# Performance work log

Measured on AMD Instinct MI355X. Metric: run time of the kernel, lower is better.

Reference implementation:

```python
import jax, jax.numpy as jnp
import numpy as np

L, B, S, H = 2, 32, 2048, 256  # layers, batch, seqlen, hidden (=input_size)


def setup_inputs() -> dict:
    key = jax.random.key(0)
    k0, k1, k2, k3, k4 = jax.random.split(key, 5)
    scale = 1.0 / np.sqrt(H)
    inputs = jax.random.normal(k0, (B, S, H), jnp.float32)
    W_ih = jax.random.uniform(k1, (L, 4 * H, H), jnp.float32, -scale, scale)
    b_ih = jax.random.uniform(k2, (L, 4 * H), jnp.float32, -scale, scale)
    W_hh = jax.random.uniform(k3, (L, 4 * H, H), jnp.float32, -scale, scale)
    b_hh = jax.random.uniform(k4, (L, 4 * H), jnp.float32, -scale, scale)
    return {"inputs": inputs, "W_ih": W_ih, "b_ih": b_ih, "W_hh": W_hh, "b_hh": b_hh}


def _lstm_layer(x, Wi, bi, Wh, bh):
    # Precompute input projection for the whole sequence (matches cells[l].ih(prev_layer)).
    xp = jnp.einsum('bsh,gh->bsg', x, Wi) + bi  # [B, S, 4H]
    hid = Wh.shape[1]
    h0 = jnp.zeros((x.shape[0], hid), x.dtype)
    c0 = jnp.zeros((x.shape[0], hid), x.dtype)

    def step(carry, xt):
        h, c = carry
        gates = xt + h @ Wh.T + bh          # [B, 4H]
        i, f, g, o = jnp.split(gates, 4, axis=-1)
        c = jax.nn.sigmoid(f) * c + jax.nn.sigmoid(i) * jnp.tanh(g)
        h = jax.nn.sigmoid(o) * jnpp_tanh(c) if False else jax.nn.sigmoid(o) * jnp.tanh(c)
        return (h, c), h

    (hT, cT), ys = jax.lax.scan(step, (h0, c0), jnp.swapaxes(xp, 0, 1))  # scan over time
    return jnp.swapaxes(ys, 0, 1), hT, cT  # [B, S, H], [B, H], [B, H]


def reference(inputs, W_ih, b_ih, W_hh, b_hh):
    # Eval-mode forward: locked dropout is identity; hiddens initialized to zeros.
    x = inputs
    hs, cs = [], []
    for l in range(W_ih.shape[0]):
        x, hT, cT = _lstm_layer(x, W_ih[l], b_ih[l], W_hh[l], b_hh[l])
        hs.append(hT)
        cs.append(cT)
    # outputs [B,S,H]; final hiddens each [L,B,H]
    return x, jnp.stack(hs, axis=0), jnp.stack(cs, axis=0)
```

## Files before the change

kernel.cpp:

```cpp
#include <hip/hip_runtime.h>
#include <cstdint>
#include <cstddef>

typedef _Float16 half_t;
typedef _Float16 half2_t __attribute__((ext_vector_type(2)));
typedef _Float16 half8_t __attribute__((ext_vector_type(8)));
typedef float   float4_t __attribute__((ext_vector_type(4)));

#define L_N 2
#define B_N 32
#define S_N 2048
#define H_N 256
#define G_N 1024
#define M_N (B_N*S_N)

#define RING_R 4
#define RING_BYTES (B_N*RING_R*128*8)

#define WS_A0   0ull
#define WS_XP   33554432ull
#define WS_WI   167772160ull
#define WS_WH   168820736ull
#define WS_BSUM 169869312ull
#define WS_HP0  169877504ull
#define WS_HP1  170008576ull

__global__ void cvt_f32_f16(const float* __restrict__ in, half_t* __restrict__ out, int n){
  int i = blockIdx.x*256 + threadIdx.x;
  if (i < n) out[i] = (half_t)in[i];
}

__global__ void make_bsum(const float* __restrict__ bi, const float* __restrict__ bh,
                          float* __restrict__ bs, int n){
  int i = blockIdx.x*256 + threadIdx.x;
  if (i < n) bs[i] = bi[i] + bh[i];
}

__global__ __launch_bounds__(256) void gemm_xp(
    const half_t* __restrict__ A, const half_t* __restrict__ W,
    const float* __restrict__ bsum, half_t* __restrict__ XP)
{
  const int wave = threadIdx.x >> 6;
  const int lane = threadIdx.x & 63;
  const int l15 = lane & 15, quad = lane >> 4;
  const int m0 = blockIdx.x*64 + wave*16;
  const int n0 = blockIdx.y*64;
  float4_t acc[4] = {{0,0,0,0},{0,0,0,0},{0,0,0,0},{0,0,0,0}};
  const half_t* arow = A + (size_t)(m0 + l15)*H_N + quad*8;
  const half_t* brow[4];
  #pragma unroll
  for (int nt=0; nt<4; ++nt)
    brow[nt] = W + (size_t)(n0 + nt*16 + l15)*H_N + quad*8;
  #pragma unroll
  for (int k0=0; k0<H_N; k0+=32){
    half8_t af = *(const half8_t*)(arow + k0);
    #pragma unroll
    for (int nt=0; nt<4; ++nt){
      half8_t bf = *(const half8_t*)(brow[nt] + k0);
      acc[nt] = __builtin_amdgcn_mfma_f32_16x16x32_f16(af, bf, acc[nt], 0, 0, 0);
    }
  }
  #pragma unroll
  for (int nt=0; nt<4; ++nt){
    const int col = n0 + nt*16 + l15;
    const int cell = col & 255, gate = col >> 8;
    const float bs = bsum[col];
    #pragma unroll
    for (int r=0; r<4; ++r){
      XP[(size_t)(m0 + quad*4 + r)*G_N + cell*4 + gate] = (half_t)(acc[nt][r] + bs);
    }
  }
}

__device__ __forceinline__ float sigf(float x){ return 1.f/(1.f + __expf(-x)); }
__device__ __forceinline__ float tanh_f(float x){ return 1.f - 2.f/(__expf(2.f*x) + 1.f); }

__device__ __forceinline__ unsigned long long ring_poll(
    const unsigned long long* p, unsigned long long tag)
{
  unsigned long long v;
  do { v = __hip_atomic_load(p, __ATOMIC_RELAXED, __HIP_MEMORY_SCOPE_AGENT); }
  while ((v >> 32) != tag);
  return v;
}

__global__ __launch_bounds__(768) void lstm_fused(
    const uint32_t* __restrict__ Wh0,
    const uint32_t* __restrict__ Wh1,
    const uint32_t* __restrict__ Wi1,
    const half_t*  __restrict__ xp,
    const float*   __restrict__ bsum1,
    unsigned long long* __restrict__ hp0,
    unsigned long long* __restrict__ hp1,
    float* __restrict__ out,
    float* __restrict__ hT, float* __restrict__ cT)
{
  __shared__ __align__(16) uint32_t h0s[128];
  __shared__ __align__(16) uint32_t h1s[128];
  __shared__ float red[6][128];
  const int tid = threadIdx.x;
  const int part = tid >> 7;
  const int r    = tid & 127;
  const int kh   = part & 1;
  const int b  = blockIdx.x & 31;
  const int s  = blockIdx.x >> 5;
  const int g  = r >> 5;
  const int cl = r & 31;
  const int cell = s*32 + cl;

  const uint32_t* wbase =
      (part < 2 ? Wh0 : (part < 4 ? Wh1 : Wi1)) + (size_t)(g*256 + cell)*128 + kh*64;
  uint32_t w[64];
  #pragma unroll
  for (int i=0;i<64;++i) w[i] = wbase[i];

  unsigned long long* r0 = hp0 + (size_t)b*(RING_R*128);
  unsigned long long* r1 = hp1 + (size_t)b*(RING_R*128);
  const size_t base = (size_t)b * S_N;

  float cst = 0.f;
  float bias0=0.f, bias1=0.f, bias2=0.f, bias3=0.f;
  if (tid >= 32 && tid < 64){
    const int mc = s*32 + (tid - 32);
    bias0 = bsum1[      mc];
    bias1 = bsum1[256 + mc];
    bias2 = bsum1[512 + mc];
    bias3 = bsum1[768 + mc];
  }

  for (int t=0; t<=S_N; ++t){
    uint2 xv = {0u,0u};
    if (tid < 32 && t < S_N)
      xv = *(const uint2*)(xp + (base + t)*G_N + (size_t)(s*32 + tid)*4);
    if (tid < 128){
      if (t > 0){
        const unsigned long long v =
            ring_poll(r0 + (size_t)((t-1)&(RING_R-1))*128 + tid,
                      (unsigned long long)(unsigned)t);
        h0s[tid] = (uint32_t)v;
      } else h0s[tid] = 0u;
    } else if (tid < 256){
      const int j = tid - 128;
      if (t > 1){
        const unsigned long long v =
            ring_poll(r1 + (size_t)((t-2)&(RING_R-1))*128 + j,
                      (unsigned long long)(unsigned)(t-1));
        h1s[j] = (uint32_t)v;
      } else h1s[j] = 0u;
    }
    __syncthreads();

    const bool active = (part < 2) ? (t < S_N) : (t >= 1);
    if (active){
      const uint32_t* hsrc = (part == 2 || part == 3) ? h1s : h0s;
      const uint4* h4 = (const uint4*)(hsrc + kh*64);
      float a0=0.f,a1=0.f,a2=0.f,a3=0.f;
      #pragma unroll
      for (int i=0;i<16;++i){
        const uint4 hh = h4[i];
        a0 = __builtin_amdgcn_fdot2(__builtin_bit_cast(half2_t, w[4*i+0]), __builtin_bit_cast(half2_t, hh.x), a0, false);
        a1 = __builtin_amdgcn_fdot2(__builtin_bit_cast(half2_t, w[4*i+1]), __builtin_bit_cast(half2_t, hh.y), a1, false);
        a2 = __builtin_amdgcn_fdot2(__builtin_bit_cast(half2_t, w[4*i+2]), __builtin_bit_cast(half2_t, hh.z), a2, false);
        a3 = __builtin_amdgcn_fdot2(__builtin_bit_cast(half2_t, w[4*i+3]), __builtin_bit_cast(half2_t, hh.w), a3, false);
      }
      red[part][r] = (a0+a1)+(a2+a3);
    }
    __syncthreads();

    if (tid < 64){
      const int half = tid >> 5;
      const int l = tid & 31;
      const int mc = s*32 + l;
      const bool act = half ? (t >= 1) : (t < S_N);
      if (act){
        float s0,s1,s2,s3;
        if (!half){
          const half2_t xlo = __builtin_bit_cast(half2_t, xv.x);
          const half2_t xhi = __builtin_bit_cast(half2_t, xv.y);
          s0 = red[0][     l] + red[1][     l] + (float)xlo.x;
          s1 = red[0][32 + l] + red[1][32 + l] + (float)xlo.y;
          s2 = red[0][64 + l] + red[1][64 + l] + (float)xhi.x;
          s3 = red[0][96 + l] + red[1][96 + l] + (float)xhi.y;
        } else {
          s0 = red[2][     l] + red[3][     l] + red[4][     l] + red[5][     l] + bias0;
          s1 = red[2][32 + l] + red[3][32 + l] + red[4][32 + l] + red[5][32 + l] + bias1;
          s2 = red[2][64 + l] + red[3][64 + l] + red[4][64 + l] + red[5][64 + l] + bias2;
          s3 = red[2][96 + l] + red[3][96 + l] + red[4][96 + l] + red[5][96 + l] + bias3;
        }
        const float gi = sigf(s0);
        const float gf = sigf(s1);
        const float gg = tanh_f(s2);
        const float go = sigf(s3);
        cst = gf*cst + gi*gg;
        const float h = go * tanh_f(cst);
        const half_t hv = (half_t)h;

        const int hu = (int)__builtin_bit_cast(unsigned short, hv);
        const int base2 = (tid & 32) | ((tid & 15) << 1);
        const int plo = __shfl(hu, base2,     64);
        const int phi = __shfl(hu, base2 + 1, 64);
        if (l < 16){
          const unsigned tag = half ? (unsigned)t : (unsigned)(t+1);
          const unsigned long long val =
              ((unsigned long long)tag << 32)
            | (unsigned long long)((((unsigned)phi & 0xffffu) << 16) | ((unsigned)plo & 0xffffu));
          unsigned long long* dst = half
            ? r1 + (size_t)((t-1)&(RING_R-1))*128 + s*16 + l
            : r0 + (size_t)( t   &(RING_R-1))*128 + s*16 + l;
          __hip_atomic_store(dst, val, __ATOMIC_RELAXED, __HIP_MEMORY_SCOPE_AGENT);
        }
        if (half){
          out[(base + (t-1))*H_N + mc] = h;
          if (t-1 == S_N-1){ hT[B_N*H_N + b*H_N + mc] = h; cT[B_N*H_N + b*H_N + mc] = cst; }
        } else {
          if (t == S_N-1){ hT[b*H_N + mc] = h; cT[b*H_N + mc] = cst; }
        }
      }
    }
  }
}

extern "C" void kernel_launch(void* const* d_in, const int* in_sizes, int n_in,
                              void* d_out, int out_size, void* d_ws, size_t ws_size,
                              hipStream_t stream)
{
  const float* x   = (const float*)d_in[0];
  const float* Wih = (const float*)d_in[1];
  const float* bih = (const float*)d_in[2];
  const float* Whh = (const float*)d_in[3];
  const float* bhh = (const float*)d_in[4];
  float* out = (float*)d_out;

  char* ws = (char*)d_ws;
  half_t* A0   = (half_t*)(ws + WS_A0);
  half_t* XP   = (half_t*)(ws + WS_XP);
  half_t* Wi16 = (half_t*)(ws + WS_WI);
  half_t* Wh16 = (half_t*)(ws + WS_WH);
  float*  bsum = (float*)(ws + WS_BSUM);
  unsigned long long* hp0 = (unsigned long long*)(ws + WS_HP0);
  unsigned long long* hp1 = (unsigned long long*)(ws + WS_HP1);

  cvt_f32_f16<<<dim3(M_N*H_N/256), dim3(256), 0, stream>>>(x, A0, M_N*H_N);
  cvt_f32_f16<<<dim3(L_N*G_N*H_N/256), dim3(256), 0, stream>>>(Wih, Wi16, L_N*G_N*H_N);
  cvt_f32_f16<<<dim3(L_N*G_N*H_N/256), dim3(256), 0, stream>>>(Whh, Wh16, L_N*G_N*H_N);
  make_bsum<<<dim3(L_N*G_N/256), dim3(256), 0, stream>>>(bih, bhh, bsum, L_N*G_N);

  float* hT = out + (size_t)M_N*H_N;
  float* cT = hT + (size_t)L_N*B_N*H_N;

  gemm_xp<<<dim3(M_N/64, G_N/64), dim3(256), 0, stream>>>(A0, Wi16, bsum, XP);

  hipMemsetAsync(hp0, 0, 2*RING_BYTES, stream);

  lstm_fused<<<dim3(B_N*8), dim3(768), 0, stream>>>(
      (const uint32_t*)Wh16,
      (const uint32_t*)(Wh16 + (size_t)G_N*H_N),
      (const uint32_t*)(Wi16 + (size_t)G_N*H_N),
      XP, bsum + G_N, hp0, hp1, out, hT, cT);
}
```

Baseline: 4.273 ms.

## Restructure LSTM step to per-wave cell ownership with shuffle reductions and one barrier

```diff
diff --git a/kernel.cpp b/kernel.cpp
--- a/kernel.cpp
+++ b/kernel.cpp
@@ -75,13 +75,19 @@
 __device__ __forceinline__ float sigf(float x){ return 1.f/(1.f + __expf(-x)); }
 __device__ __forceinline__ float tanh_f(float x){ return 1.f - 2.f/(__expf(2.f*x) + 1.f); }
 
-__device__ __forceinline__ unsigned long long ring_poll(
-    const unsigned long long* p, unsigned long long tag)
-{
-  unsigned long long v;
-  do { v = __hip_atomic_load(p, __ATOMIC_RELAXED, __HIP_MEMORY_SCOPE_AGENT); }
-  while ((v >> 32) != tag);
-  return v;
+__device__ __forceinline__ uint32_t ring_poll(const unsigned long long* p, unsigned tag){
+  unsigned long long a = __hip_atomic_load(p, __ATOMIC_RELAXED, __HIP_MEMORY_SCOPE_AGENT);
+  for (;;){
+    unsigned long long b = __hip_atomic_load(p, __ATOMIC_RELAXED, __HIP_MEMORY_SCOPE_AGENT);
+    if ((unsigned)(a >> 32) == tag) return (uint32_t)a;
+    a = b;
+  }
+}
+
+__device__ __forceinline__ void wg_barrier_lds(){
+  asm volatile("s_waitcnt lgkmcnt(0)" ::: "memory");
+  __builtin_amdgcn_s_barrier();
+  asm volatile("" ::: "memory");
 }
 
 __global__ __launch_bounds__(768) void lstm_fused(
@@ -95,125 +101,155 @@
     float* __restrict__ out,
     float* __restrict__ hT, float* __restrict__ cT)
 {
-  __shared__ __align__(16) uint32_t h0s[128];
-  __shared__ __align__(16) uint32_t h1s[128];
-  __shared__ float red[6][128];
+  __shared__ __align__(16) uint32_t hcat[2][256];
   const int tid = threadIdx.x;
-  const int part = tid >> 7;
-  const int r    = tid & 127;
-  const int kh   = part & 1;
-  const int b  = blockIdx.x & 31;
-  const int s  = blockIdx.x >> 5;
-  const int g  = r >> 5;
-  const int cl = r & 31;
-  const int cell = s*32 + cl;
-
-  const uint32_t* wbase =
-      (part < 2 ? Wh0 : (part < 4 ? Wh1 : Wi1)) + (size_t)(g*256 + cell)*128 + kh*64;
-  uint32_t w[64];
-  #pragma unroll
-  for (int i=0;i<64;++i) w[i] = wbase[i];
+  const int wv  = tid >> 6;
+  const int l   = tid & 63;
+  const int b   = blockIdx.x & 31;
+  const int s   = blockIdx.x >> 5;
+  const bool isL0 = (wv < 4);
+
+  const int cw   = isL0 ? (l >> 3) : (l >> 4);
+  const int kl   = isL0 ? (l & 7)  : (l & 15);
+  const int cell = isL0 ? (s*32 + wv*8 + cw) : (s*32 + (wv-4)*4 + cw);
+  const int hbase = isL0 ? (128 + kl*16) : (kl*16);
+
+  uint4 wreg[4][4];
+  {
+    const uint32_t* mat; int koff;
+    if (isL0)      { mat = Wh0; koff = kl*16; }
+    else if (kl<8) { mat = Wh1; koff = kl*16; }
+    else           { mat = Wi1; koff = (kl-8)*16; }
+    #pragma unroll
+    for (int p=0;p<4;++p){
+      const uint32_t* rp = mat + (size_t)(p*256 + cell)*128 + koff;
+      #pragma unroll
+      for (int i=0;i<4;++i) wreg[p][i] = *(const uint4*)(rp + 4*i);
+    }
+  }
+
+  float bb0=0.f, bb1=0.f, bb2=0.f, bb3=0.f;
+  if (!isL0 && kl==0){
+    bb0 = bsum1[      cell];
+    bb1 = bsum1[256 + cell];
+    bb2 = bsum1[512 + cell];
+    bb3 = bsum1[768 + cell];
+  }
 
   unsigned long long* r0 = hp0 + (size_t)b*(RING_R*128);
   unsigned long long* r1 = hp1 + (size_t)b*(RING_R*128);
   const size_t base = (size_t)b * S_N;
-
   float cst = 0.f;
-  float bias0=0.f, bias1=0.f, bias2=0.f, bias3=0.f;
-  if (tid >= 32 && tid < 64){
-    const int mc = s*32 + (tid - 32);
-    bias0 = bsum1[      mc];
-    bias1 = bsum1[256 + mc];
-    bias2 = bsum1[512 + mc];
-    bias3 = bsum1[768 + mc];
-  }
 
   for (int t=0; t<=S_N; ++t){
     uint2 xv = {0u,0u};
-    if (tid < 32 && t < S_N)
-      xv = *(const uint2*)(xp + (base + t)*G_N + (size_t)(s*32 + tid)*4);
-    if (tid < 128){
-      if (t > 0){
-        const unsigned long long v =
-            ring_poll(r0 + (size_t)((t-1)&(RING_R-1))*128 + tid,
-                      (unsigned long long)(unsigned)t);
-        h0s[tid] = (uint32_t)v;
-      } else h0s[tid] = 0u;
-    } else if (tid < 256){
-      const int j = tid - 128;
-      if (t > 1){
-        const unsigned long long v =
-            ring_poll(r1 + (size_t)((t-2)&(RING_R-1))*128 + j,
-                      (unsigned long long)(unsigned)(t-1));
-        h1s[j] = (uint32_t)v;
-      } else h1s[j] = 0u;
-    }
-    __syncthreads();
-
-    const bool active = (part < 2) ? (t < S_N) : (t >= 1);
+    if (isL0 && kl==0 && t < S_N)
+      xv = *(const uint2*)(xp + (base+t)*G_N + (size_t)cell*4);
+
+    const int bufi = t & 1;
+    if (wv < 2){
+      const int a = wv*64 + l;
+      uint32_t hv = 0u;
+      if (t > 0) hv = ring_poll(r0 + (size_t)((t-1)&(RING_R-1))*128 + a, (unsigned)t);
+      hcat[bufi][128 + a] = hv;
+    } else if (wv < 4){
+      const int a = (wv-2)*64 + l;
+      uint32_t hv = 0u;
+      if (t > 1) hv = ring_poll(r1 + (size_t)((t-2)&(RING_R-1))*128 + a, (unsigned)(t-1));
+      hcat[bufi][a] = hv;
+    }
+    wg_barrier_lds();
+
+    const bool active = isL0 ? (t < S_N) : (t >= 1);
     if (active){
-      const uint32_t* hsrc = (part == 2 || part == 3) ? h1s : h0s;
-      const uint4* h4 = (const uint4*)(hsrc + kh*64);
-      float a0=0.f,a1=0.f,a2=0.f,a3=0.f;
+      const uint4* hsrc = (const uint4*)&hcat[bufi][hbase];
+      const uint4 hh0 = hsrc[0], hh1 = hsrc[1], hh2 = hsrc[2], hh3 = hsrc[3];
+
+      float gate[4];
       #pragma unroll
-      for (int i=0;i<16;++i){
-        const uint4 hh = h4[i];
-        a0 = __builtin_amdgcn_fdot2(__builtin_bit_cast(half2_t, w[4*i+0]), __builtin_bit_cast(half2_t, hh.x), a0, false);
-        a1 = __builtin_amdgcn_fdot2(__builtin_bit_cast(half2_t, w[4*i+1]), __builtin_bit_cast(half2_t, hh.y), a1, false);
-        a2 = __builtin_amdgcn_fdot2(__builtin_bit_cast(half2_t, w[4*i+2]), __builtin_bit_cast(half2_t, hh.z), a2, false);
-        a3 = __builtin_amdgcn_fdot2(__builtin_bit_cast(half2_t, w[4*i+3]), __builtin_bit_cast(half2_t, hh.w), a3, false);
+      for (int p=0;p<4;++p){
+        float a0=0.f,a1=0.f,a2=0.f,a3=0.f;
+        {
+          const uint4 ww = wreg[p][0];
+          a0 = __builtin_amdgcn_fdot2(__builtin_bit_cast(half2_t, ww.x), __builtin_bit_cast(half2_t, hh0.x), a0, false);
+          a1 = __builtin_amdgcn_fdot2(__builtin_bit_cast(half2_t, ww.y), __builtin_bit_cast(half2_t, hh0.y), a1, false);
+          a2 = __builtin_amdgcn_fdot2(__builtin_bit_cast(half2_t, ww.z), __builtin_bit_cast(half2_t, hh0.z), a2, false);
+          a3 = __builtin_amdgcn_fdot2(__builtin_bit_cast(half2_t, ww.w), __builtin_bit_cast(half2_t, hh0.w), a3, false);
+        }
+        {
+          const uint4 ww = wreg[p][1];
+          a0 = __builtin_amdgcn_fdot2(__builtin_bit_cast(half2_t, ww.x), __builtin_bit_cast(half2_t, hh1.x), a0, false);
+          a1 = __builtin_amdgcn_fdot2(__builtin_bit_cast(half2_t, ww.y), __builtin_bit_cast(half2_t, hh1.y), a1, false);
+          a2 = __builtin_amdgcn_fdot2(__builtin_bit_cast(half2_t, ww.z), __builtin_bit_cast(half2_t, hh1.z), a2, false);
+          a3 = __builtin_amdgcn_fdot2(__builtin_bit_cast(half2_t, ww.w), __builtin_bit_cast(half2_t, hh1.w), a3, false);
+        }
+        {
+          const uint4 ww = wreg[p][2];
+          a0 = __builtin_amdgcn_fdot2(__builtin_bit_cast(half2_t, ww.x), __builtin_bit_cast(half2_t, hh2.x), a0, false);
+          a1 = __builtin_amdgcn_fdot2(__builtin_bit_cast(half2_t, ww.y), __builtin_bit_cast(half2_t, hh2.y), a1, false);
+          a2 = __builtin_amdgcn_fdot2(__builtin_bit_cast(half2_t, ww.z), __builtin_bit_cast(half2_t, hh2.z), a2, false);
+          a3 = __builtin_amdgcn_fdot2(__builtin_bit_cast(half2_t, ww.w), __builtin_bit_cast(half2_t, hh2.w), a3, false);
+        }
+        {
+          const uint4 ww = wreg[p][3];
+          a0 = __builtin_amdgcn_fdot2(__builtin_bit_cast(half2_t, ww.x), __builtin_bit_cast(half2_t, hh3.x), a0, false);
+          a1 = __builtin_amdgcn_fdot2(__builtin_bit_cast(half2_t, ww.y), __builtin_bit_cast(half2_t, hh3.y), a1, false);
+          a2 = __builtin_amdgcn_fdot2(__builtin_bit_cast(half2_t, ww.z), __builtin_bit_cast(half2_t, hh3.z), a2, false);
+          a3 = __builtin_amdgcn_fdot2(__builtin_bit_cast(half2_t, ww.w), __builtin_bit_cast(half2_t, hh3.w), a3, false);
+        }
+        float v = (a0+a1)+(a2+a3);
+        v += __shfl_xor(v, 1, 64);
+        v += __shfl_xor(v, 2, 64);
+        v += __shfl_xor(v, 4, 64);
+        if (!isL0) v += __shfl_xor(v, 8, 64);
+        gate[p] = v;
       }
-      red[part][r] = (a0+a1)+(a2+a3);
-    }
-    __syncthreads();
-
-    if (tid < 64){
-      const int half = tid >> 5;
-      const int l = tid & 31;
-      const int mc = s*32 + l;
-      const bool act = half ? (t >= 1) : (t < S_N);
-      if (act){
-        float s0,s1,s2,s3;
-        if (!half){
-          const half2_t xlo = __builtin_bit_cast(half2_t, xv.x);
-          const half2_t xhi = __builtin_bit_cast(half2_t, xv.y);
-          s0 = red[0][     l] + red[1][     l] + (float)xlo.x;
-          s1 = red[0][32 + l] + red[1][32 + l] + (float)xlo.y;
-          s2 = red[0][64 + l] + red[1][64 + l] + (float)xhi.x;
-          s3 = red[0][96 + l] + red[1][96 + l] + (float)xhi.y;
-        } else {
-          s0 = red[2][     l] + red[3][     l] + red[4][     l] + red[5][     l] + bias0;
-          s1 = red[2][32 + l] + red[3][32 + l] + red[4][32 + l] + red[5][32 + l] + bias1;
-          s2 = red[2][64 + l] + red[3][64 + l] + red[4][64 + l] + red[5][64 + l] + bias2;
-          s3 = red[2][96 + l] + red[3][96 + l] + red[4][96 + l] + red[5][96 + l] + bias3;
-        }
-        const float gi = sigf(s0);
-        const float gf = sigf(s1);
-        const float gg = tanh_f(s2);
-        const float go = sigf(s3);
-        cst = gf*cst + gi*gg;
-        const float h = go * tanh_f(cst);
-        const half_t hv = (half_t)h;
-
-        const int hu = (int)__builtin_bit_cast(unsigned short, hv);
-        const int base2 = (tid & 32) | ((tid & 15) << 1);
-        const int plo = __shfl(hu, base2,     64);
-        const int phi = __shfl(hu, base2 + 1, 64);
-        if (l < 16){
-          const unsigned tag = half ? (unsigned)t : (unsigned)(t+1);
+
+      float s0,s1,s2,s3;
+      if (isL0){
+        const half2_t xlo = __builtin_bit_cast(half2_t, xv.x);
+        const half2_t xhi = __builtin_bit_cast(half2_t, xv.y);
+        s0 = gate[0] + (float)xlo.x;
+        s1 = gate[1] + (float)xlo.y;
+        s2 = gate[2] + (float)xhi.x;
+        s3 = gate[3] + (float)xhi.y;
+      } else {
+        s0 = gate[0] + bb0; s1 = gate[1] + bb1;
+        s2 = gate[2] + bb2; s3 = gate[3] + bb3;
+      }
+      const float gi = sigf(s0);
+      const float gf = sigf(s1);
+      const float gg = tanh_f(s2);
+      const float go = sigf(s3);
+      cst = gf*cst + gi*gg;
+      const float h = go * tanh_f(cst);
+      const half_t hv16 = (half_t)h;
+      const int hu = (int)__builtin_bit_cast(unsigned short, hv16);
+
+      if (isL0){
+        const int phi = __shfl(hu, (l + 8) & 63, 64);
+        if ((l & 15) == 0){
+          const int j = l >> 4;
           const unsigned long long val =
-              ((unsigned long long)tag << 32)
-            | (unsigned long long)((((unsigned)phi & 0xffffu) << 16) | ((unsigned)plo & 0xffffu));
-          unsigned long long* dst = half
-            ? r1 + (size_t)((t-1)&(RING_R-1))*128 + s*16 + l
-            : r0 + (size_t)( t   &(RING_R-1))*128 + s*16 + l;
-          __hip_atomic_store(dst, val, __ATOMIC_RELAXED, __HIP_MEMORY_SCOPE_AGENT);
-        }
-        if (half){
-          out[(base + (t-1))*H_N + mc] = h;
-          if (t-1 == S_N-1){ hT[B_N*H_N + b*H_N + mc] = h; cT[B_N*H_N + b*H_N + mc] = cst; }
-        } else {
-          if (t == S_N-1){ hT[b*H_N + mc] = h; cT[b*H_N + mc] = cst; }
+              ((unsigned long long)(unsigned)(t+1) << 32)
+            | (unsigned long long)((((unsigned)phi & 0xffffu) << 16) | ((unsigned)hu & 0xffffu));
+          __hip_atomic_store(r0 + (size_t)(t&(RING_R-1))*128 + s*16 + wv*4 + j, val,
+                             __ATOMIC_RELAXED, __HIP_MEMORY_SCOPE_AGENT);
+        }
+        if (kl == 0 && t == S_N-1){ hT[b*H_N + cell] = h; cT[b*H_N + cell] = cst; }
+      } else {
+        const int phi = __shfl(hu, (l + 16) & 63, 64);
+        if ((l & 31) == 0){
+          const int j = l >> 5;
+          const unsigned long long val =
+              ((unsigned long long)(unsigned)t << 32)
+            | (unsigned long long)((((unsigned)phi & 0xffffu) << 16) | ((unsigned)hu & 0xffffu));
+          __hip_atomic_store(r1 + (size_t)((t-1)&(RING_R-1))*128 + s*16 + (wv-4)*2 + j, val,
+                             __ATOMIC_RELAXED, __HIP_MEMORY_SCOPE_AGENT);
+        }
+        if (kl == 0){
+          out[(base + (t-1))*H_N + cell] = h;
+          if (t == S_N){ hT[B_N*H_N + b*H_N + cell] = h; cT[B_N*H_N + b*H_N + cell] = cst; }
         }
       }
     }
```

After: 8.123 ms. 1.9x slower.
